# Optimization experiments

Hardware: AMD Instinct MI355X
Metric: run time of the kernel (lower is better)

The kernel has to match this reference:

```python
import jax, jax.numpy as jnp
import numpy as np

H = 4  # num_heads

def _ln(x, g, b):
    m = x.mean(-1, keepdims=True)
    v = ((x - m) ** 2).mean(-1, keepdims=True)
    return (x - m) * jax.lax.rsqrt(v + 1e-5) * g + b

def _mlp(x, w1, b1, w2, b2):
    return jax.nn.relu(x @ w1 + b1) @ w2 + b2

def _lin_att(q, k, v):
    # q,k,v: [BB, L, H, hd] ; linear (kernelized) attention, no softmax
    L = q.shape[1]
    qn = q / jnp.maximum(jnp.linalg.norm(q, axis=-1, keepdims=True), 1e-12)
    kn = k / jnp.maximum(jnp.linalg.norm(k, axis=-1, keepdims=True), 1e-12)
    kvs = jnp.einsum('blhm,blhd->bhmd', kn, v)
    num = jnp.einsum('bnhm,bhmd->bnhd', qn, kvs) + L * v
    den = jnp.einsum('bnhm,bhm->bnh', qn, kn.sum(axis=1))[..., None] + L
    return num / den

def _fast_attn(x4, w_qkv, w_op, b_op):
    # x4: [B,T,N,D]; spatial attention over N, temporal attention over T, concat, project
    B, T, N, D = x4.shape
    hd = D // H
    q, k, v = jnp.split(x4 @ w_qkv, 3, axis=-1)
    sh = lambda t: t.reshape(B * T, N, H, hd)
    out_s = _lin_att(sh(q), sh(k), sh(v)).reshape(B, T, N, D)
    th = lambda t: jnp.swapaxes(t, 1, 2).reshape(B * N, T, H, hd)
    out_t = jnp.swapaxes(_lin_att(th(q), th(k), th(v)).reshape(B, N, T, D), 1, 2)
    return jnp.concatenate([out_s, out_t], axis=-1) @ w_op + b_op

def _forward(x, W_in, b_in, adp, W_tp, b_tp, qkv_w, op_w, op_b, pw_w, pw_b,
             fc_w1, fc_b1, fc_w2, fc_b2, ln1_g, ln1_b, ln2_g, ln2_b,
             ep_w, ep_b, enc_w1, enc_b1, enc_w2, enc_b2, out_w, out_b):
    Nn, T, _ = x.shape
    xt = jnp.swapaxes(x, 0, 1)[None]                 # [1,T,N,in]
    h = xt @ W_in + b_in                             # input_proj -> [1,T,N,24]
    h = jnp.concatenate([h, adp[None]], axis=-1)     # + adaptive emb -> [1,T,N,104]
    h = h @ W_tp + b_tp                              # temporal_proj: 1x1 conv == pointwise linear
    graph = jnp.einsum('tnd,tmd->tnm', adp, adp)     # [T,N,N]
    graph = jax.nn.softmax(jax.nn.relu(graph), axis=-1)  # AvgPool(1,1) is identity
    # GraphPropagate (order=2, eval/no-dropout): [h, graph @ h]
    z1 = jnp.einsum('tni,btid->btnd', graph, h)
    att0 = _fast_attn(h, qkv_w[0], op_w[0], op_b[0])
    att1 = _fast_attn(z1, qkv_w[1], op_w[1], op_b[1])
    # scale = [1, 0.01]; note torch's in-place aliasing makes ln1 input = 2*x_glo
    g = h + att0 * (h @ pw_w[0] + pw_b[0]) + 0.01 * att1 * (att0 @ pw_w[1] + pw_b[1])
    h1 = _ln(2.0 * g, ln1_g, ln1_b)
    h2 = _ln(h1 + _mlp(h1, fc_w1, fc_b1, fc_w2, fc_b2), ln2_g, ln2_b)
    y = jnp.swapaxes(h2, 1, 2).reshape(1, Nn, T * h2.shape[-1]) @ ep_w + ep_b  # encoder_proj
    for i in range(enc_w1.shape[0]):                 # 3 residual MLP blocks
        y = y + _mlp(y, enc_w1[i], enc_b1[i], enc_w2[i], enc_b2[i])
    out = y @ out_w + out_b                          # [1,N,365]
    return out.reshape(Nn, T, 1)

def setup_inputs() -> dict:
    key = jax.random.key(0)
    ks = jax.random.split(key, 24)
    f = lambda i, shape, s=0.05: jax.random.normal(ks[i], shape, dtype=jnp.float32) * s
    D, T, N, IN = 104, 365, 400, 3
    return {
        'x': jax.random.normal(ks[0], (N, T, IN), dtype=jnp.float32),
        'W_in': f(1, (IN, 24)), 'b_in': f(2, (24,)),
        'adp': f(3, (T, N, 80)),
        'W_tp': f(4, (D, D)), 'b_tp': f(5, (D,)),
        'qkv_w': f(6, (2, D, 3 * D)),
        'op_w': f(7, (2, 2 * D, D)), 'op_b': f(8, (2, D)),
        'pw_w': f(9, (2, D, D)), 'pw_b': f(10, (2, D)),
        'fc_w1': f(11, (D, 2 * D)), 'fc_b1': f(12, (2 * D,)),
        'fc_w2': f(13, (2 * D, D)), 'fc_b2': f(14, (D,)),
        'ln1_g': jnp.ones((D,), jnp.float32), 'ln1_b': jnp.zeros((D,), jnp.float32),
        'ln2_g': jnp.ones((D,), jnp.float32), 'ln2_b': jnp.zeros((D,), jnp.float32),
        'ep_w': f(15, (T * D, D), 0.01), 'ep_b': f(16, (D,)),
        'enc_w1': f(17, (3, D, 2 * D)), 'enc_b1': f(18, (3, 2 * D)),
        'enc_w2': f(19, (3, 2 * D, D)), 'enc_b2': f(20, (3, D)),
        'out_w': f(21, (D, T)), 'out_b': f(22, (T,)),
    }

def reference(x, W_in, b_in, adp, W_tp, b_tp, qkv_w, op_w, op_b, pw_w, pw_b,
              fc_w1, fc_b1, fc_w2, fc_b2, ln1_g, ln1_b, ln2_g, ln2_b,
              ep_w, ep_b, enc_w1, enc_b1, enc_w2, enc_b2, out_w, out_b):
    return _forward(x, W_in, b_in, adp, W_tp, b_tp, qkv_w, op_w, op_b, pw_w, pw_b,
                    fc_w1, fc_b1, fc_w2, fc_b2, ln1_g, ln1_b, ln2_g, ln2_b,
                    ep_w, ep_b, enc_w1, enc_b1, enc_w2, enc_b2, out_w, out_b)
```

## Files before the change

### kernel.cpp

```cpp
#include <hip/hip_runtime.h>
#include <hip/hip_bf16.h>
#include <cstddef>

#define TT   365
#define NN   400
#define TN   (TT*NN)
#define HD   26
#define NH   4

#define CEILDIV(a,b) (((a)+(b)-1)/(b))

typedef __hip_bfloat16 bf16;
typedef short short8v __attribute__((ext_vector_type(8)));
typedef float float4v __attribute__((ext_vector_type(4)));
typedef float float16v __attribute__((ext_vector_type(16)));
__device__ __forceinline__ float b2f(bf16 v){ return __bfloat162float(v); }
__device__ __forceinline__ bf16  f2b(float v){ return __float2bfloat16(v); }

static constexpr size_t NB0 = (size_t)TN*104;
static constexpr size_t NB1 = (size_t)TN*104;
static constexpr size_t NB2 = (size_t)TN*312;
static constexpr size_t NB3 = (size_t)TN*104;
static constexpr size_t NBF = NB0+NB1+NB2+NB3;
static constexpr size_t NTILE   = (size_t)108*32;
// ... 190 lines not shown
    int m0 = blockIdx.x * 64;
    int tid = threadIdx.x;
    int lane = tid & 63, w = tid >> 6, n16 = lane & 15, quad = lane >> 4;
    uint4 z4 = {0u,0u,0u,0u};

    for (int idx = tid; idx < 64*16; idx += 256) {
        int r = idx >> 4, q = idx & 15;
        int m = m0 + r;
        uint4 v0 = z4, v1 = z4;
        if (m < TN && q < 13) {
            v0 = *(const uint4*)(h    + (size_t)m*104 + q*8);
            v1 = *(const uint4*)(att0 + (size_t)m*104 + q*8);
        }
        *(uint4*)(&A0s[r*STR + q*8]) = v0;
        *(uint4*)(&A1s[r*STR + q*8]) = v1;
    }
    for (int idx = tid; idx < 112*16; idx += 256) {
        int c = idx >> 4, q = idx & 15;
        uint4 v = z4;
        if (c < 104) v = *(const uint4*)(w0t + (size_t)c*128 + q*8);
        *(uint4*)(&Ws[c*STR + q*8]) = v;
    }
    for (int i = tid; i < 416; i += 256)
        prm[i] = (i < 208) ? pwb[i] : (i < 312 ? gamma[i-208] : beta[i-312]);
    __syncthreads();

    short8v a0f[4], a1f[4];
    #pragma unroll
    for (int s = 0; s < 4; ++s) {
        a0f[s] = *(const short8v*)(&A0s[(16*w + n16)*STR + s*32 + quad*8]);
        a1f[s] = *(const short8v*)(&A1s[(16*w + n16)*STR + s*32 + quad*8]);
    }
    float4v acc0[7], acc1[7];
    #pragma unroll
    for (int ct = 0; ct < 7; ++ct) { float4v z = {0.f,0.f,0.f,0.f}; acc0[ct] = z; acc1[ct] = z; }
    #pragma unroll
    for (int ct = 0; ct < 7; ++ct)
        #pragma unroll
        for (int s = 0; s < 4; ++s) {
            short8v bfr = *(const short8v*)(&Ws[(ct*16 + n16)*STR + s*32 + quad*8]);
            acc0[ct] = __builtin_amdgcn_mfma_f32_16x16x32_bf16(a0f[s], bfr, acc0[ct], 0, 0, 0);
        }
    __syncthreads();
    for (int idx = tid; idx < 112*16; idx += 256) {
        int c = idx >> 4, q = idx & 15;
        uint4 v = z4;
        if (c < 104) v = *(const uint4*)(w1t + (size_t)c*128 + q*8);
        *(uint4*)(&Ws[c*STR + q*8]) = v;
    }
    __syncthreads();
    #pragma unroll
    for (int ct = 0; ct < 7; ++ct)
        #pragma unroll
        for (int s = 0; s < 4; ++s) {
            short8v bfr = *(const short8v*)(&Ws[(ct*16 + n16)*STR + s*32 + quad*8]);
            acc1[ct] = __builtin_amdgcn_mfma_f32_16x16x32_bf16(a1f[s], bfr, acc1[ct], 0, 0, 0);
        }

    float sum[4] = {0.f,0.f,0.f,0.f};
    #pragma unroll
    for (int ct = 0; ct < 7; ++ct) {
        int c = ct*16 + n16;
        bool colok = c < 104;
        float b0 = colok ? prm[c] : 0.f;
        float b1 = colok ? prm[104 + c] : 0.f;
        #pragma unroll
        for (int reg = 0; reg < 4; ++reg) {
            int r = 16*w + quad*4 + reg;
            int m = m0 + r;
            float xv = 0.f;
            if (colok && m < TN) {
                float p0 = acc0[ct][reg] + b0;
                float p1 = acc1[ct][reg] + b1;
                float hv = b2f(A0s[r*STR + c]);
                float a0 = b2f(A1s[r*STR + c]);
                float a1 = b2f(att1[(size_t)m*104 + c]);
                xv = 2.f*(hv + a0*p0 + 0.01f*a1*p1);
            }
            acc0[ct][reg] = xv;
            sum[reg] += xv;
        }
    }
    #pragma unroll
    for (int reg = 0; reg < 4; ++reg) {
        float v = sum[reg];
        v += __shfl_xor(v,1,64); v += __shfl_xor(v,2,64);
        v += __shfl_xor(v,4,64); v += __shfl_xor(v,8,64);
        sum[reg] = v * (1.f/104.f);
    }
    float var[4] = {0.f,0.f,0.f,0.f};
    #pragma unroll
    for (int ct = 0; ct < 7; ++ct) {
        bool colok = (ct*16 + n16) < 104;
        #pragma unroll
        for (int reg = 0; reg < 4; ++reg) {
            if (colok) {
                float d = acc0[ct][reg] - sum[reg];
                acc0[ct][reg] = d;
                var[reg] += d*d;
            }
        }
    }
    #pragma unroll
    for (int reg = 0; reg < 4; ++reg) {
        float v = var[reg];
        v += __shfl_xor(v,1,64); v += __shfl_xor(v,2,64);
        v += __shfl_xor(v,4,64); v += __shfl_xor(v,8,64);
        var[reg] = rsqrtf(v * (1.f/104.f) + 1e-5f);
    }
    #pragma unroll
    for (int ct = 0; ct < 7; ++ct) {
        int c = ct*16 + n16;
        if (c < 104) {
            float g = prm[208 + c], be = prm[312 + c];
            #pragma unroll
            for (int reg = 0; reg < 4; ++reg) {
                int m = m0 + 16*w + quad*4 + reg;
                if (m < TN)
                    h[(size_t)m*104 + c] = f2b(acc0[ct][reg]*var[reg]*g + be);
            }
        }
    }
}

__global__ void __launch_bounds__(256) fc2_ln2(
    const bf16* __restrict__ hidden, const bf16* __restrict__ w2t, const float* __restrict__ b2,
    const bf16* __restrict__ h1, const float* __restrict__ gamma, const float* __restrict__ beta,
    bf16* __restrict__ h2)
{
    constexpr int STRA = 232;
    constexpr int STRW = 136;
    __shared__ bf16 As[64*STRA];
    __shared__ bf16 Ws[112*STRW];
    __shared__ float prm[312];
    int m0 = blockIdx.x * 64;
    int tid = threadIdx.x;
    int lane = tid & 63, w = tid >> 6, n16 = lane & 15, quad = lane >> 4;
    uint4 z4 = {0u,0u,0u,0u};

    for (int idx = tid; idx < 64*28; idx += 256) {
        int r = idx / 28, q = idx - r*28;
        int m = m0 + r;
        uint4 v = z4;
        if (m < TN && q < 26) v = *(const uint4*)(hidden + (size_t)m*208 + q*8);
        *(uint4*)(&As[r*STRA + q*8]) = v;
    }
    for (int idx = tid; idx < 112*16; idx += 256) {
        int c = idx >> 4, q = idx & 15;
        uint4 v = z4;
        if (c < 104) v = *(const uint4*)(w2t + (size_t)c*224 + q*8);
        *(uint4*)(&Ws[c*STRW + q*8]) = v;
    }
    for (int i = tid; i < 312; i += 256)
        prm[i] = (i < 104) ? b2[i] : (i < 208 ? gamma[i-104] : beta[i-208]);
    __syncthreads();

    short8v af[7];
    #pragma unroll
    for (int s = 0; s < 7; ++s)
        af[s] = *(const short8v*)(&As[(16*w + n16)*STRA + s*32 + quad*8]);
    float4v acc[7];
    #pragma unroll
    for (int ct = 0; ct < 7; ++ct) { float4v z = {0.f,0.f,0.f,0.f}; acc[ct] = z; }
    #pragma unroll
    for (int ct = 0; ct < 7; ++ct)
        #pragma unroll
        for (int s = 0; s < 4; ++s) {
            short8v bfr = *(const short8v*)(&Ws[(ct*16 + n16)*STRW + s*32 + quad*8]);
            acc[ct] = __builtin_amdgcn_mfma_f32_16x16x32_bf16(af[s], bfr, acc[ct], 0, 0, 0);
        }
    __syncthreads();
    for (int idx = tid; idx < 112*16; idx += 256) {
        int c = idx >> 4, q = idx & 15;
        uint4 v = z4;
        if (c < 104 && q < 12) v = *(const uint4*)(w2t + (size_t)c*224 + 128 + q*8);
        *(uint4*)(&Ws[c*STRW + q*8]) = v;
    }
    __syncthreads();
    #pragma unroll
    for (int ct = 0; ct < 7; ++ct)
        #pragma unroll
        for (int s = 4; s < 7; ++s) {
            short8v bfr = *(const short8v*)(&Ws[(ct*16 + n16)*STRW + (s-4)*32 + quad*8]);
            acc[ct] = __builtin_amdgcn_mfma_f32_16x16x32_bf16(af[s], bfr, acc[ct], 0, 0, 0);
        }

    float sum[4] = {0.f,0.f,0.f,0.f};
    #pragma unroll
    for (int ct = 0; ct < 7; ++ct) {
        int c = ct*16 + n16;
        bool colok = c < 104;
        float bb = colok ? prm[c] : 0.f;
        #pragma unroll
        for (int reg = 0; reg < 4; ++reg) {
            int m = m0 + 16*w + quad*4 + reg;
            float xv = 0.f;
            if (colok && m < TN)
                xv = b2f(h1[(size_t)m*104 + c]) + acc[ct][reg] + bb;
            acc[ct][reg] = xv;
            sum[reg] += xv;
        }
    }
    #pragma unroll
    for (int reg = 0; reg < 4; ++reg) {
        float v = sum[reg];
        v += __shfl_xor(v,1,64); v += __shfl_xor(v,2,64);
        v += __shfl_xor(v,4,64); v += __shfl_xor(v,8,64);
        sum[reg] = v * (1.f/104.f);
    }
    float var[4] = {0.f,0.f,0.f,0.f};
    #pragma unroll
    for (int ct = 0; ct < 7; ++ct) {
        bool colok = (ct*16 + n16) < 104;
        #pragma unroll
        for (int reg = 0; reg < 4; ++reg) {
            if (colok) {
                float d = acc[ct][reg] - sum[reg];
                acc[ct][reg] = d;
                var[reg] += d*d;
            }
        }
    }
    #pragma unroll
    for (int reg = 0; reg < 4; ++reg) {
        float v = var[reg];
        v += __shfl_xor(v,1,64); v += __shfl_xor(v,2,64);
        v += __shfl_xor(v,4,64); v += __shfl_xor(v,8,64);
        var[reg] = rsqrtf(v * (1.f/104.f) + 1e-5f);
    }
    #pragma unroll
    for (int ct = 0; ct < 7; ++ct) {
        int c = ct*16 + n16;
        if (c < 104) {
            float g = prm[104 + c], be = prm[208 + c];
            #pragma unroll
            for (int reg = 0; reg < 4; ++reg) {
                int m = m0 + 16*w + quad*4 + reg;
                if (m < TN)
                    h2[(size_t)m*104 + c] = f2b(acc[ct][reg]*var[reg]*g + be);
            }
        }
    }
}

__global__ void __launch_bounds__(256) ep_mf(
    const bf16* __restrict__ h2, const bf16* __restrict__ wt, float* __restrict__ y)
{
    constexpr int STR = 136;
    __shared__ bf16 As[64*STR];
    __shared__ bf16 Ws[64*STR];
    int m0 = blockIdx.x * 64;
    int c0 = blockIdx.y * 64;
    int t0 = blockIdx.z * 8;
    int t1 = min(TT, t0 + 8);
    int tid = threadIdx.x;
    int lane = tid & 63, w = tid >> 6, n16 = lane & 15, quad = lane >> 4;
    uint4 z4 = {0u,0u,0u,0u};

    float4v acc[4];
    #pragma unroll
    for (int ct = 0; ct < 4; ++ct) { float4v z = {0.f,0.f,0.f,0.f}; acc[ct] = z; }

    for (int t = t0; t < t1; ++t) {
        for (int idx = tid; idx < 64*16; idx += 256) {
            int r = idx >> 4, q = idx & 15;
            int m = m0 + r;
            uint4 va = z4;
            if (m < NN && q < 13) va = *(const uint4*)(h2 + ((size_t)t*NN + m)*104 + q*8);
            *(uint4*)(&As[r*STR + q*8]) = va;
            int c = c0 + r;
            uint4 vw = z4;
            if (c < 104 && q < 13) vw = *(const uint4*)(wt + (size_t)c*37960 + t*104 + q*8);
            *(uint4*)(&Ws[r*STR + q*8]) = vw;
        }
        __syncthreads();
        short8v af[4];
        #pragma unroll
        for (int s = 0; s < 4; ++s)
            af[s] = *(const short8v*)(&As[(16*w + n16)*STR + s*32 + quad*8]);
        #pragma unroll
        for (int ct = 0; ct < 4; ++ct) {
            #pragma unroll
            for (int s = 0; s < 4; ++s) {
                short8v bfr = *(const short8v*)(&Ws[(ct*16 + n16)*STR + s*32 + quad*8]);
                acc[ct] = __builtin_amdgcn_mfma_f32_16x16x32_bf16(af[s], bfr, acc[ct], 0, 0, 0);
            }
        }
        __syncthreads();
    }
    #pragma unroll
    for (int ct = 0; ct < 4; ++ct) {
        int c = c0 + ct*16 + n16;
        if (c < 104) {
            #pragma unroll
            for (int reg = 0; reg < 4; ++reg) {
                int m = m0 + 16*w + quad*4 + reg;
                if (m < NN) atomicAdd(&y[(size_t)m*104 + c], acc[ct][reg]);
            }
        }
    }
}

static constexpr int Z1_TQ = CEILDIV(TT, 8);
static constexpr int Z1_BLOCKS = 8 * Z1_TQ * 7;
__global__ void __launch_bounds__(256, 3) z1_mf(
    const bf16* __restrict__ adp_bf, const bf16* __restrict__ hT, bf16* __restrict__ z1)
{
    constexpr int SA  = 104;
    constexpr int SPH = 72;
    constexpr int SPP = 72;
    __shared__ bf16 Bt[64*SA];
    __shared__ bf16 Hs[128*SPH];
    __shared__ bf16 P [64*SPP];
    __shared__ float rsb[2][64];
    bf16* As = Hs;

    int bid = blockIdx.x;
    int xcd = bid & 7;
    int j = bid >> 3;
    int tq = j / 7, rblk = j - tq*7;
    int t = tq*8 + xcd;
    if (t >= TT) return;
    int r0 = rblk*64;

    int tid = threadIdx.x;
    int lane = tid & 63, w = tid >> 6;
    int n32 = lane & 31, koct = lane >> 5;
    int qi = w >> 1, ci = w & 1;

    {
        const uint4* src = (const uint4*)(adp_bf + ((size_t)t*NN + r0)*96);
        for (int idx = tid; idx < 768; idx += 256) {
            int r = idx / 12, q = idx - r*12;
            *(uint4*)(&As[r*SA + q*8]) = src[idx];
        }
    }
    __syncthreads();
    short8v af2[6];
    #pragma unroll
    for (int s = 0; s < 6; ++s)
        af2[s] = *(const short8v*)(&As[(qi*32 + n32)*SA + s*16 + koct*8]);
    __syncthreads();
    {
        uint4 z4v = {0u,0u,0u,0u};
        for (int idx = tid; idx < 216; idx += 256) {
            int r = 104 + idx/9, q = idx - (idx/9)*9;
            *(uint4*)(&Hs[r*SPH + q*8]) = z4v;
        }
    }

    float16v onum0, onum1;
    #pragma unroll
    for (int i = 0; i < 16; ++i) { onum0[i] = 0.f; onum1[i] = 0.f; }
    float rs2[16];
    #pragma unroll
    for (int i = 0; i < 16; ++i) rs2[i] = 0.f;

    uint4 preB[3], preH[4];
    {
        const uint4* srcB = (const uint4*)(adp_bf + (size_t)t*NN*96);
        #pragma unroll
        for (int j2 = 0; j2 < 3; ++j2) preB[j2] = srcB[tid + j2*256];
        const bf16* hb = hT + (size_t)t*104*448;
        #pragma unroll
        for (int j2 = 0; j2 < 4; ++j2) {
            int idx = tid + j2*256;
            uint4 v = {0u,0u,0u,0u};
            if (idx < 832) {
                int d = idx >> 3, q = idx & 7;
                v = *(const uint4*)(hb + (size_t)d*448 + q*8);
            }
            preH[j2] = v;
        }
    }

    for (int c0 = 0; c0 < NN; c0 += 64) {
        #pragma unroll
        for (int j2 = 0; j2 < 3; ++j2) {
            int idx = tid + j2*256;
            int r = idx / 12, q = idx - r*12;
            *(uint4*)(&Bt[r*SA + q*8]) = preB[j2];
        }
        #pragma unroll
        for (int j2 = 0; j2 < 4; ++j2) {
            int idx = tid + j2*256;
            if (idx < 832) {
                int d = idx >> 3, q = idx & 7;
                *(uint4*)(&Hs[d*SPH + q*8]) = preH[j2];
            }
        }
        __syncthreads();
        int cn = c0 + 64;
        if (cn < NN) {
            const uint4* srcB = (const uint4*)(adp_bf + ((size_t)t*NN + cn)*96);
            #pragma unroll
            for (int j2 = 0; j2 < 3; ++j2) preB[j2] = srcB[tid + j2*256];
            const bf16* hb = hT + (size_t)t*104*448 + cn;
            #pragma unroll
            for (int j2 = 0; j2 < 4; ++j2) {
                int idx = tid + j2*256;
                if (idx < 832) {
                    int d = idx >> 3, q = idx & 7;
                    preH[j2] = *(const uint4*)(hb + (size_t)d*448 + q*8);
                }
            }
        }
        float16v sc;
        #pragma unroll
        for (int i = 0; i < 16; ++i) sc[i] = 0.f;
        #pragma unroll
        for (int s = 0; s < 6; ++s) {
            short8v bfr = *(const short8v*)(&Bt[(ci*32 + n32)*SA + s*16 + koct*8]);
            sc = __builtin_amdgcn_mfma_f32_32x32x16_bf16(af2[s], bfr, sc, 0, 0, 0);
        }
        bool colok = (c0 + ci*32 + n32) < NN;
        #pragma unroll
        for (int reg = 0; reg < 16; ++reg) {
            int crow = (reg & 3) + 8*(reg >> 2) + 4*koct;
            float e = colok ? __expf(fmaxf(sc[reg], 0.f)) : 0.f;
            rs2[reg] += e;
            P[(qi*32 + crow)*SPP + ci*32 + n32] = f2b(e);
        }
        __syncthreads();
        short8v pA[4];
        #pragma unroll
        for (int s = 0; s < 4; ++s)
            pA[s] = *(const short8v*)(&P[(qi*32 + n32)*SPP + s*16 + koct*8]);
        int dt0 = (w & 1), dt1 = dt0 + 2;
        #pragma unroll
        for (int s = 0; s < 4; ++s) {
            short8v hb0 = *(const short8v*)(&Hs[(dt0*32 + n32)*SPH + s*16 + koct*8]);
            onum0 = __builtin_amdgcn_mfma_f32_32x32x16_bf16(pA[s], hb0, onum0, 0, 0, 0);
        }
        #pragma unroll
        for (int s = 0; s < 4; ++s) {
            short8v hb1 = *(const short8v*)(&Hs[(dt1*32 + n32)*SPH + s*16 + koct*8]);
            onum1 = __builtin_amdgcn_mfma_f32_32x32x16_bf16(pA[s], hb1, onum1, 0, 0, 0);
        }
        __syncthreads();
    }

    #pragma unroll
    for (int reg = 0; reg < 16; ++reg) {
        float v = rs2[reg];
        v += __shfl_xor(v, 1, 64);
        v += __shfl_xor(v, 2, 64);
        v += __shfl_xor(v, 4, 64);
        v += __shfl_xor(v, 8, 64);
        v += __shfl_xor(v, 16, 64);
        if (n32 == 0) {
            int crow = (reg & 3) + 8*(reg >> 2) + 4*koct;
            rsb[ci][qi*32 + crow] = v;
        }
    }
    __syncthreads();

    int dt0 = (w & 1), dt1 = dt0 + 2;
    #pragma unroll
    for (int reg = 0; reg < 16; ++reg) {
        int crow = (reg & 3) + 8*(reg >> 2) + 4*koct;
        int qrow = qi*32 + crow;
        int gq = r0 + qrow;
        if (gq < NN) {
            float inv = 1.f / (rsb[0][qrow] + rsb[1][qrow]);
            int d0 = dt0*32 + n32;
            z1[((size_t)t*NN + gq)*104 + d0] = f2b(onum0[reg] * inv);
            int d1 = dt1*32 + n32;
            if (d1 < 104)
                z1[((size_t)t*NN + gq)*104 + d1] = f2b(onum1[reg] * inv);
        }
    }
}

__global__ void __launch_bounds__(256) kvs_mf(
    const bf16* __restrict__ qkv, bf16* __restrict__ kvsb_s, bf16* __restrict__ kvsb_t)
{
    constexpr int CK = 32;
    constexpr int TS = 40;
    __shared__ bf16 raw[CK][216];
    __shared__ bf16 kTn[4][32][TS];
    __shared__ bf16 vT [4][32][TS];
    __shared__ float invs[CK][4];

    int bb = blockIdx.x;
    bf16* out; int L; long long strideL, base;
    if (bb < TT) { out = kvsb_s + (size_t)bb*NTILE; L = NN; base = (long long)bb*NN*312 + 104; strideL = 312; }
    else { int n = bb - TT; out = kvsb_t + (size_t)n*NTILE; L = TT; base = (long long)n*312 + 104; strideL = (long long)NN*312; }

    int tid = threadIdx.x;
    int lane = tid & 63, w = tid >> 6;
    int n32 = lane & 31, koct = lane >> 5;
    uint4 z4 = {0u,0u,0u,0u};

    float16v acc;
    #pragma unroll
    for (int i = 0; i < 16; ++i) acc[i] = 0.f;

    uint4 pre[4];
    #pragma unroll
    for (int j = 0; j < 4; ++j) {
        int idx = tid + j*256;
        uint4 v = z4;
        if (idx < CK*26) {
            int r = idx / 26, q = idx - r*26;
            if (r < L) v = *(const uint4*)(qkv + base + (long long)r*strideL + q*8);
        }
        pre[j] = v;
    }

    for (int l0 = 0; l0 < L; l0 += CK) {
        int lw = min(CK, L - l0);
        __syncthreads();
        #pragma unroll
        for (int j = 0; j < 4; ++j) {
            int idx = tid + j*256;
            if (idx < CK*26) {
                int r = idx / 26, q = idx - r*26;
                *(uint4*)(&raw[r][q*8]) = pre[j];
            }
        }
        __syncthreads();
        {
            int ln0 = l0 + CK;
            #pragma unroll
            for (int j = 0; j < 4; ++j) {
                int idx = tid + j*256;
                uint4 v = z4;
                if (idx < CK*26 && ln0 < L) {
                    int r = idx / 26, q = idx - r*26;
                    if (r < L - ln0) v = *(const uint4*)(qkv + base + (long long)(ln0 + r)*strideL + q*8);
                }
                pre[j] = v;
            }
        }
        if (tid < CK*4) {
            int l = tid >> 2, h = tid & 3;
            float ss = 0.f;
            #pragma unroll
            for (int m = 0; m < HD; ++m) { float v = b2f(raw[l][h*HD + m]); ss += v*v; }
            invs[l][h] = (l < lw) ? 1.f/fmaxf(sqrtf(ss), 1e-12f) : 0.f;
        }
        __syncthreads();
        for (int idx = tid; idx < 4*CK*HD; idx += 256) {
            int h = idx / (CK*HD); int rem = idx - h*CK*HD;
            int l = rem / HD; int m = rem - l*HD;
            float iv = invs[l][h];
            kTn[h][m][l] = f2b(b2f(raw[l][h*HD + m]) * iv);
            vT[h][m][l]  = raw[l][104 + h*HD + m];
        }
        if (tid < 4*CK) {
            int h = tid >> 5, l = tid & 31;
            vT[h][26][l] = f2b((l < lw) ? 1.f : 0.f);
        }
        __syncthreads();
        #pragma unroll
        for (int s = 0; s < 2; ++s) {
            short8v a = *(const short8v*)(&kTn[w][n32][s*16 + koct*8]);
            short8v b = *(const short8v*)(&vT [w][n32][s*16 + koct*8]);
            acc = __builtin_amdgcn_mfma_f32_32x32x16_bf16(a, b, acc, 0, 0, 0);
        }
    }

    int lo = w*HD;
    #pragma unroll
    for (int reg = 0; reg < 16; ++reg) {
        int m = (reg & 3) + 8*(reg >> 2) + 4*koct;
        if (m < HD) {
            if (n32 < HD)       out[(size_t)(lo + n32)*32 + m] = f2b(acc[reg]);
            else if (n32 == HD) out[(size_t)(104 + w)*32 + m] = f2b(acc[reg]);
        }
    }
}

__global__ void __launch_bounds__(256) attn_mm(
    bf16* __restrict__ qkv, const bf16* __restrict__ kvsb,
    int M, long long bStride, long long rowStride, float Lf, int outOff)
{
    constexpr int STR = 136;
    __shared__ bf16 As[64*STR];
    __shared__ bf16 Ws[112*STR];
    __shared__ float nsqL[64*4];
    __shared__ float denL[64*4];
    int mt = blockIdx.x, bb = blockIdx.y;
    int tid = threadIdx.x;
    int lane = tid & 63, w = tid >> 6, n16 = lane & 15, quad = lane >> 4;
    bf16* base = qkv + (size_t)bb * bStride;
    int r0 = mt*64;
    uint4 z4 = {0u,0u,0u,0u};

    for (int idx = tid; idx < 64*16; idx += 256) {
        int r = idx >> 4, q = idx & 15;
        int m = r0 + r;
        uint4 v = z4;
        if (m < M && q < 13) v = *(const uint4*)(base + (size_t)m*rowStride + q*8);
        *(uint4*)(&As[r*STR + q*8]) = v;
    }
    for (int idx = tid; idx < 112*16; idx += 256) {
        int c = idx >> 4, q = idx & 15;
        *(uint4*)(&Ws[c*STR + q*8]) = z4;
    }
    __syncthreads();
    {
        const bf16* kb = kvsb + (size_t)bb * NTILE;
        for (int idx = tid; idx < 108*13; idx += 256) {
            int c = idx / 13, qu = idx - c*13;
            int lo = (c < 104) ? (c/26)*26 : (c-104)*26;
            *(uint*)(&Ws[c*STR + lo + qu*2]) = *(const uint*)(kb + (size_t)c*32 + qu*2);
        }
    }
    __syncthreads();

    short8v af[4];
    #pragma unroll
    for (int s = 0; s < 4; ++s)
        af[s] = *(const short8v*)(&As[(16*w + n16)*STR + s*32 + quad*8]);
    float4v acc[7];
    #pragma unroll
    for (int ct = 0; ct < 7; ++ct) { float4v z = {0.f,0.f,0.f,0.f}; acc[ct] = z; }
    #pragma unroll
    for (int ct = 0; ct < 7; ++ct) {
        #pragma unroll
        for (int s = 0; s < 4; ++s) {
            short8v bfr = *(const short8v*)(&Ws[(ct*16 + n16)*STR + s*32 + quad*8]);
            acc[ct] = __builtin_amdgcn_mfma_f32_16x16x32_bf16(af[s], bfr, acc[ct], 0, 0, 0);
        }
    }
    {
        int row = tid >> 2, hh = tid & 3;
        const bf16* qr = &As[row*STR + hh*26];
        float ss = 0.f;
        #pragma unroll
        for (int m = 0; m < HD; ++m) { float v = b2f(qr[m]); ss += v*v; }
        nsqL[row*4 + hh] = ss;
    }
    if (n16 >= 8 && n16 < 12) {
        #pragma unroll
        for (int reg = 0; reg < 4; ++reg)
            denL[(16*w + quad*4 + reg)*4 + (n16 - 8)] = acc[6][reg];
    }
    __syncthreads();
    #pragma unroll
    for (int ct = 0; ct < 7; ++ct) {
        int c = ct*16 + n16;
        if (c < 104) {
            int hh = c / 26;
            #pragma unroll
            for (int reg = 0; reg < 4; ++reg) {
                int lr = 16*w + quad*4 + reg;
                int m = r0 + lr;
                if (m < M) {
                    float iq = 1.f / fmaxf(sqrtf(nsqL[lr*4 + hh]), 1e-12f);
                    float den = iq * denL[lr*4 + hh] + Lf;
                    bf16* rp = base + (size_t)m*rowStride;
                    float num = iq * acc[ct][reg] + Lf * b2f(rp[208 + c]);
                    rp[outOff + c] = f2b(num / den);
                }
            }
        }
    }
}

__global__ void __launch_bounds__(256) y_init_kernel(float* __restrict__ y, const float* __restrict__ ep_b) {
    int i = blockIdx.x*256 + threadIdx.x;
    if (i < NN*104) y[i] = ep_b[i % 104];
}

__global__ void __launch_bounds__(256) enc_kernel(
    float* __restrict__ y, const float* __restrict__ w1, const float* __restrict__ b1,
    const float* __restrict__ w2, const float* __restrict__ b2)
{
    int n = blockIdx.x;
    int tid = threadIdx.x;
    __shared__ float yr[104], hid[208];
    if (tid < 104) yr[tid] = y[(size_t)n*104 + tid];
    __syncthreads();
    if (tid < 208) {
        float s = b1[tid];
        for (int k = 0; k < 104; ++k) s += yr[k] * w1[(size_t)k*208 + tid];
        hid[tid] = fmaxf(s, 0.f);
    }
    __syncthreads();
    if (tid < 104) {
        float s = b2[tid];
        for (int k = 0; k < 208; ++k) s += hid[k] * w2[(size_t)k*104 + tid];
        y[(size_t)n*104 + tid] = yr[tid] + s;
    }
}

__global__ void __launch_bounds__(256) out_kernel(
    const float* __restrict__ y, const float* __restrict__ out_w,
    const float* __restrict__ out_b, float* __restrict__ out)
{
    int n = blockIdx.x;
    int tid = threadIdx.x;
    __shared__ float yr[104];
    if (tid < 104) yr[tid] = y[(size_t)n*104 + tid];
    __syncthreads();
    for (int t = tid; t < TT; t += 256) {
        float s = out_b[t];
        for (int d = 0; d < 104; ++d) s += yr[d] * out_w[(size_t)d*TT + t];
        out[(size_t)n*TT + t] = s;
    }
}

extern "C" void kernel_launch(void* const* d_in, const int* in_sizes, int n_in,
                              void* d_out, int out_size, void* d_ws, size_t ws_size,
                              hipStream_t stream) {
    if (ws_size < WS_NEEDED) return;

    const float* x      = (const float*)d_in[0];
    const float* W_in   = (const float*)d_in[1];
    const float* b_in   = (const float*)d_in[2];
    const float* adp    = (const float*)d_in[3];
    const float* W_tp   = (const float*)d_in[4];
    const float* b_tp   = (const float*)d_in[5];
    const float* qkv_w  = (const float*)d_in[6];
    const float* op_w   = (const float*)d_in[7];
    const float* op_b   = (const float*)d_in[8];
    const float* pw_w   = (const float*)d_in[9];
    const float* pw_b   = (const float*)d_in[10];
    const float* fc_w1  = (const float*)d_in[11];
    const float* fc_b1  = (const float*)d_in[12];
    const float* fc_w2  = (const float*)d_in[13];
    const float* fc_b2  = (const float*)d_in[14];
    const float* ln1_g  = (const float*)d_in[15];
    const float* ln1_b  = (const float*)d_in[16];
    const float* ln2_g  = (const float*)d_in[17];
    const float* ln2_b  = (const float*)d_in[18];
    const float* ep_w   = (const float*)d_in[19];
    const float* ep_b   = (const float*)d_in[20];
    const float* enc_w1 = (const float*)d_in[21];
    const float* enc_b1 = (const float*)d_in[22];
    const float* enc_w2 = (const float*)d_in[23];
    const float* enc_b2 = (const float*)d_in[24];
    const float* out_w  = (const float*)d_in[25];
    const float* out_b  = (const float*)d_in[26];

    bf16* B0 = (bf16*)d_ws;
    bf16* B1 = B0 + NB0;
    bf16* B2 = B1 + NB1;
    bf16* B3 = B2 + NB2;
    bf16* kvsb_s = B3 + NB3;
    bf16* kvsb_t = kvsb_s + NKVSB_S;
    float* ybuf  = (float*)(kvsb_t + NKVSB_T);
    bf16* wtp   = (bf16*)(ybuf + NY);
    bf16* wqkv0 = wtp + NW_TP;
    bf16* wqkv1 = wqkv0 + NW_QKV;
    bf16* wop0  = wqkv1 + NW_QKV;
    bf16* wop1  = wop0 + NW_OP;
    bf16* wpw0  = wop1 + NW_OP;
    bf16* wpw1  = wpw0 + NW_PW;
    bf16* wfc1  = wpw1 + NW_PW;
    bf16* wfc2  = wfc1 + NW_FC1;
    bf16* wept  = wfc2 + NW_FC2;
    bf16* adp_bf = B2;
    bf16* hTbuf  = B2 + NADP;

    prep_w<<<CEILDIV(104*128,256), 256, 0, stream>>>(W_tp, wtp, 104, 104, 128);
    prep_w<<<CEILDIV(312*128,256), 256, 0, stream>>>(qkv_w, wqkv0, 104, 312, 128);
    prep_w<<<CEILDIV(312*128,256), 256, 0, stream>>>(qkv_w + 104*312, wqkv1, 104, 312, 128);
    prep_w<<<CEILDIV(104*224,256), 256, 0, stream>>>(op_w, wop0, 208, 104, 224);
    prep_w<<<CEILDIV(104*224,256), 256, 0, stream>>>(op_w + 208*104, wop1, 208, 104, 224);
    prep_w<<<CEILDIV(104*128,256), 256, 0, stream>>>(pw_w, wpw0, 104, 104, 128);
    prep_w<<<CEILDIV(104*128,256), 256, 0, stream>>>(pw_w + 104*104, wpw1, 104, 104, 128);
    prep_w<<<CEILDIV(208*128,256), 256, 0, stream>>>(fc_w1, wfc1, 104, 208, 128);
    prep_w<<<CEILDIV(104*224,256), 256, 0, stream>>>(fc_w2, wfc2, 208, 104, 224);
    prep_wT<<<CEILDIV(37960,64), 256, 0, stream>>>(ep_w, wept);

    const int GX = CEILDIV(TN, 64);

    hcat_kernel<<<TN, 128, 0, stream>>>(x, W_in, b_in, adp, B2);
    gemm_mf<128><<<GX*2, 256, 0, stream>>>(B2, 104, 104, wtp, b_tp, B0, TN, 104, 0);
    prep_adp<<<CEILDIV((int)NADP,256), 256, 0, stream>>>(adp, adp_bf);
    ht_kernel<<<dim3(7, TT), 256, 0, stream>>>(B0, hTbuf);
    z1_mf<<<Z1_BLOCKS, 256, 0, stream>>>(adp_bf, hTbuf, B1);
    gemm_mf<128><<<GX*5, 256, 0, stream>>>(B0, 104, 104, wqkv0, nullptr, B2, TN, 312, 0);
    kvs_mf<<<TT+NN, 256, 0, stream>>>(B2, kvsb_s, kvsb_t);
    attn_mm<<<dim3(6, NN), 256, 0, stream>>>(B2, kvsb_t, TT, 312, (long long)NN*312, (float)TT, 104);
    attn_mm<<<dim3(7, TT), 256, 0, stream>>>(B2, kvsb_s, NN, (long long)NN*312, 312, (float)NN, 0);
    gemm_mf<224><<<GX*2, 256, 0, stream>>>(B2, 312, 208, wop0, op_b, B3, TN, 104, 0);
    gemm_mf<128><<<GX*5, 256, 0, stream>>>(B1, 104, 104, wqkv1, nullptr, B2, TN, 312, 0);
    kvs_mf<<<TT+NN, 256, 0, stream>>>(B2, kvsb_s, kvsb_t);
    attn_mm<<<dim3(6, NN), 256, 0, stream>>>(B2, kvsb_t, TT, 312, (long long)NN*312, (float)TT, 104);
    attn_mm<<<dim3(7, TT), 256, 0, stream>>>(B2, kvsb_s, NN, (long long)NN*312, 312, (float)NN, 0);
    gemm_mf<224><<<GX*2, 256, 0, stream>>>(B2, 312, 208, wop1, op_b + 104, B1, TN, 104, 0);
    gate_ln1<<<GX, 256, 0, stream>>>(B0, B3, B1, wpw0, wpw1, pw_b, ln1_g, ln1_b);
    gemm_mf<128><<<GX*4, 256, 0, stream>>>(B0, 104, 104, wfc1, fc_b1, B2, TN, 208, 1);
    fc2_ln2<<<GX, 256, 0, stream>>>(B2, wfc2, fc_b2, B0, ln2_g, ln2_b, B3);
    y_init_kernel<<<CEILDIV(NN*104,256), 256, 0, stream>>>(ybuf, ep_b);
    ep_mf<<<dim3(CEILDIV(NN,64), 2, CEILDIV(TT,8)), 256, 0, stream>>>(B3, wept, ybuf);
    for (int i = 0; i < 3; ++i)
        enc_kernel<<<NN, 256, 0, stream>>>(ybuf, enc_w1 + (size_t)i*104*208, enc_b1 + (size_t)i*208,
                                           enc_w2 + (size_t)i*208*104, enc_b2 + (size_t)i*104);
    out_kernel<<<NN, 256, 0, stream>>>(ybuf, out_w, out_b, (float*)d_out);
}
```

Baseline: 1.320 ms.

## Split z1 graph-propagate kernel over feature halves and keep P in registers

The z1 kernel now splits the 104-wide output feature dimension into two halves across separate blocks, doubling the grid and raising the occupancy hint to 4. The score MFMA is transposed so the exp'd probabilities can be packed to bf16 and rearranged with permlane32 swaps directly into A-operand registers. This removes the P round-trip through LDS and one barrier per tile. Waves now split the key dimension and reduce partial outputs through shared memory at the end. The cost is recomputing the QK^T scores and exponentials twice (once per half).

```diff
diff --git a/kernel.cpp b/kernel.cpp
--- a/kernel.cpp
+++ b/kernel.cpp
@@ -516,22 +516,23 @@
 }
 
 static constexpr int Z1_TQ = CEILDIV(TT, 8);
-static constexpr int Z1_BLOCKS = 8 * Z1_TQ * 7;
-__global__ void __launch_bounds__(256, 3) z1_mf(
+static constexpr int Z1_BLOCKS = 8 * Z1_TQ * 7 * 2;
+__global__ void __launch_bounds__(256, 4) z1_mf(
     const bf16* __restrict__ adp_bf, const bf16* __restrict__ hT, bf16* __restrict__ z1)
 {
-    constexpr int SA  = 104;
-    constexpr int SPH = 72;
-    constexpr int SPP = 72;
-    __shared__ bf16 Bt[64*SA];
-    __shared__ bf16 Hs[128*SPH];
-    __shared__ bf16 P [64*SPP];
-    __shared__ float rsb[2][64];
-    bf16* As = Hs;
+    constexpr int SA = 104;
+    constexpr int SH = 72;
+    __shared__ __align__(16) bf16 lds[64*SA*2 + 64*SH];
+    __shared__ float rsbp[128];
+    bf16* Asq = lds;
+    bf16* Bt  = lds + 64*SA;
+    bf16* Hs  = lds + 128*SA;
+    float* xbuf = (float*)lds;
 
     int bid = blockIdx.x;
     int xcd = bid & 7;
     int j = bid >> 3;
+    int dh = j & 1; j >>= 1;
     int tq = j / 7, rblk = j - tq*7;
     int t = tq*8 + xcd;
     if (t >= TT) return;
@@ -546,44 +547,29 @@
         const uint4* src = (const uint4*)(adp_bf + ((size_t)t*NN + r0)*96);
         for (int idx = tid; idx < 768; idx += 256) {
             int r = idx / 12, q = idx - r*12;
-            *(uint4*)(&As[r*SA + q*8]) = src[idx];
-        }
-    }
-    __syncthreads();
-    short8v af2[6];
-    #pragma unroll
-    for (int s = 0; s < 6; ++s)
-        af2[s] = *(const short8v*)(&As[(qi*32 + n32)*SA + s*16 + koct*8]);
-    __syncthreads();
-    {
-        uint4 z4v = {0u,0u,0u,0u};
-        for (int idx = tid; idx < 216; idx += 256) {
-            int r = 104 + idx/9, q = idx - (idx/9)*9;
-            *(uint4*)(&Hs[r*SPH + q*8]) = z4v;
-        }
-    }
-
-    float16v onum0, onum1;
-    #pragma unroll
-    for (int i = 0; i < 16; ++i) { onum0[i] = 0.f; onum1[i] = 0.f; }
-    float rs2[16];
-    #pragma unroll
-    for (int i = 0; i < 16; ++i) rs2[i] = 0.f;
-
-    uint4 preB[3], preH[4];
+            *(uint4*)(&Asq[r*SA + q*8]) = src[idx];
+        }
+    }
+
+    float16v on0, on1;
+    #pragma unroll
+    for (int i = 0; i < 16; ++i) { on0[i] = 0.f; on1[i] = 0.f; }
+    float rs = 0.f;
+
+    const bf16* hbase = hT + (size_t)t*104*448 + (size_t)(dh*64)*448;
+    const int hrows = (dh == 0) ? 64 : 40;
+
+    uint4 preB[3], preH[2];
     {
         const uint4* srcB = (const uint4*)(adp_bf + (size_t)t*NN*96);
         #pragma unroll
         for (int j2 = 0; j2 < 3; ++j2) preB[j2] = srcB[tid + j2*256];
-        const bf16* hb = hT + (size_t)t*104*448;
-        #pragma unroll
-        for (int j2 = 0; j2 < 4; ++j2) {
+        #pragma unroll
+        for (int j2 = 0; j2 < 2; ++j2) {
             int idx = tid + j2*256;
+            int r = idx >> 3, c8 = idx & 7;
             uint4 v = {0u,0u,0u,0u};
-            if (idx < 832) {
-                int d = idx >> 3, q = idx & 7;
-                v = *(const uint4*)(hb + (size_t)d*448 + q*8);
-            }
+            if (r < hrows) v = *(const uint4*)(hbase + (size_t)r*448 + c8*8);
             preH[j2] = v;
         }
     }
@@ -596,12 +582,10 @@
             *(uint4*)(&Bt[r*SA + q*8]) = preB[j2];
         }
         #pragma unroll
-        for (int j2 = 0; j2 < 4; ++j2) {
+        for (int j2 = 0; j2 < 2; ++j2) {
             int idx = tid + j2*256;
-            if (idx < 832) {
-                int d = idx >> 3, q = idx & 7;
-                *(uint4*)(&Hs[d*SPH + q*8]) = preH[j2];
-            }
+            int r = idx >> 3, c8 = idx & 7;
+            *(uint4*)(&Hs[r*SH + c8*8]) = preH[j2];
         }
         __syncthreads();
         int cn = c0 + 64;
@@ -609,14 +593,13 @@
             const uint4* srcB = (const uint4*)(adp_bf + ((size_t)t*NN + cn)*96);
             #pragma unroll
             for (int j2 = 0; j2 < 3; ++j2) preB[j2] = srcB[tid + j2*256];
-            const bf16* hb = hT + (size_t)t*104*448 + cn;
             #pragma unroll
-            for (int j2 = 0; j2 < 4; ++j2) {
+            for (int j2 = 0; j2 < 2; ++j2) {
                 int idx = tid + j2*256;
-                if (idx < 832) {
-                    int d = idx >> 3, q = idx & 7;
-                    preH[j2] = *(const uint4*)(hb + (size_t)d*448 + q*8);
-                }
+                int r = idx >> 3, c8 = idx & 7;
+                uint4 v = {0u,0u,0u,0u};
+                if (r < hrows) v = *(const uint4*)(hbase + (size_t)r*448 + cn + c8*8);
+                preH[j2] = v;
             }
         }
         float16v sc;
@@ -624,64 +607,66 @@
         for (int i = 0; i < 16; ++i) sc[i] = 0.f;
         #pragma unroll
         for (int s = 0; s < 6; ++s) {
-            short8v bfr = *(const short8v*)(&Bt[(ci*32 + n32)*SA + s*16 + koct*8]);
-            sc = __builtin_amdgcn_mfma_f32_32x32x16_bf16(af2[s], bfr, sc, 0, 0, 0);
-        }
-        bool colok = (c0 + ci*32 + n32) < NN;
+            short8v afc = *(const short8v*)(&Bt [(ci*32 + n32)*SA + s*16 + koct*8]);
+            short8v bq  = *(const short8v*)(&Asq[(qi*32 + n32)*SA + s*16 + koct*8]);
+            sc = __builtin_amdgcn_mfma_f32_32x32x16_bf16(afc, bq, sc, 0, 0, 0);
+        }
+        uint r8[8];
+        #pragma unroll
+        for (int i = 0; i < 8; ++i) {
+            int crow0 = (2*i & 3) + 8*(2*i >> 2) + 4*koct;
+            int cg = c0 + ci*32 + crow0;
+            float e0 = (cg     < NN) ? __expf(fmaxf(sc[2*i],   0.f)) : 0.f;
+            float e1 = (cg + 1 < NN) ? __expf(fmaxf(sc[2*i+1], 0.f)) : 0.f;
+            rs += e0 + e1;
+            asm("v_cvt_pk_bf16_f32 %0, %1, %2" : "=v"(r8[i]) : "v"(e0), "v"(e1));
+        }
+        asm volatile("v_permlane32_swap_b32 %0, %1" : "+v"(r8[2]), "+v"(r8[0]));
+        asm volatile("v_permlane32_swap_b32 %0, %1" : "+v"(r8[3]), "+v"(r8[1]));
+        asm volatile("v_permlane32_swap_b32 %0, %1" : "+v"(r8[6]), "+v"(r8[4]));
+        asm volatile("v_permlane32_swap_b32 %0, %1" : "+v"(r8[7]), "+v"(r8[5]));
+        union { uint4 u; short8v s; } cv0, cv1;
+        cv0.u.x = r8[0]; cv0.u.y = r8[1]; cv0.u.z = r8[2]; cv0.u.w = r8[3];
+        cv1.u.x = r8[4]; cv1.u.y = r8[5]; cv1.u.z = r8[6]; cv1.u.w = r8[7];
+        #pragma unroll
+        for (int s = 0; s < 2; ++s) {
+            short8v pa = (s == 0) ? cv0.s : cv1.s;
+            short8v h0 = *(const short8v*)(&Hs[(0*32 + n32)*SH + ci*32 + s*16 + koct*8]);
+            on0 = __builtin_amdgcn_mfma_f32_32x32x16_bf16(pa, h0, on0, 0, 0, 0);
+            short8v h1 = *(const short8v*)(&Hs[(1*32 + n32)*SH + ci*32 + s*16 + koct*8]);
+            on1 = __builtin_amdgcn_mfma_f32_32x32x16_bf16(pa, h1, on1, 0, 0, 0);
+        }
+        __syncthreads();
+    }
+
+    float rsl = rs + __shfl_xor(rs, 32, 64);
+    if (koct == 0) rsbp[ci*64 + qi*32 + n32] = rsl;
+    if (ci == 1) {
         #pragma unroll
         for (int reg = 0; reg < 16; ++reg) {
             int crow = (reg & 3) + 8*(reg >> 2) + 4*koct;
-            float e = colok ? __expf(fmaxf(sc[reg], 0.f)) : 0.f;
-            rs2[reg] += e;
-            P[(qi*32 + crow)*SPP + ci*32 + n32] = f2b(e);
-        }
-        __syncthreads();
-        short8v pA[4];
-        #pragma unroll
-        for (int s = 0; s < 4; ++s)
-            pA[s] = *(const short8v*)(&P[(qi*32 + n32)*SPP + s*16 + koct*8]);
-        int dt0 = (w & 1), dt1 = dt0 + 2;
-        #pragma unroll
-        for (int s = 0; s < 4; ++s) {
-            short8v hb0 = *(const short8v*)(&Hs[(dt0*32 + n32)*SPH + s*16 + koct*8]);
-            onum0 = __builtin_amdgcn_mfma_f32_32x32x16_bf16(pA[s], hb0, onum0, 0, 0, 0);
-        }
-        #pragma unroll
-        for (int s = 0; s < 4; ++s) {
-            short8v hb1 = *(const short8v*)(&Hs[(dt1*32 + n32)*SPH + s*16 + koct*8]);
-            onum1 = __builtin_amdgcn_mfma_f32_32x32x16_bf16(pA[s], hb1, onum1, 0, 0, 0);
-        }
-        __syncthreads();
-    }
-
-    #pragma unroll
-    for (int reg = 0; reg < 16; ++reg) {
-        float v = rs2[reg];
-        v += __shfl_xor(v, 1, 64);
-        v += __shfl_xor(v, 2, 64);
-        v += __shfl_xor(v, 4, 64);
-        v += __shfl_xor(v, 8, 64);
-        v += __shfl_xor(v, 16, 64);
-        if (n32 == 0) {
+            xbuf[qi*2048 +        crow*32 + n32] = on0[reg];
+            xbuf[qi*2048 + 1024 + crow*32 + n32] = on1[reg];
+        }
+    }
+    __syncthreads();
+    if (ci == 0) {
+        float rtot = rsbp[qi*32 + n32] + rsbp[64 + qi*32 + n32];
+        float inv = 1.f / rtot;
+        #pragma unroll
+        for (int reg = 0; reg < 16; ++reg) {
             int crow = (reg & 3) + 8*(reg >> 2) + 4*koct;
-            rsb[ci][qi*32 + crow] = v;
-        }
-    }
-    __syncthreads();
-
-    int dt0 = (w & 1), dt1 = dt0 + 2;
-    #pragma unroll
-    for (int reg = 0; reg < 16; ++reg) {
-        int crow = (reg & 3) + 8*(reg >> 2) + 4*koct;
-        int qrow = qi*32 + crow;
-        int gq = r0 + qrow;
-        if (gq < NN) {
-            float inv = 1.f / (rsb[0][qrow] + rsb[1][qrow]);
-            int d0 = dt0*32 + n32;
-            z1[((size_t)t*NN + gq)*104 + d0] = f2b(onum0[reg] * inv);
-            int d1 = dt1*32 + n32;
-            if (d1 < 104)
-                z1[((size_t)t*NN + gq)*104 + d1] = f2b(onum1[reg] * inv);
+            int gq = r0 + qi*32 + crow;
+            if (gq < NN) {
+                float v0 = (on0[reg] + xbuf[qi*2048 + crow*32 + n32]) * inv;
+                int d0 = dh*64 + n32;
+                z1[((size_t)t*NN + gq)*104 + d0] = f2b(v0);
+                int d1 = dh*64 + 32 + n32;
+                if (d1 < 104) {
+                    float v1 = (on1[reg] + xbuf[qi*2048 + 1024 + crow*32 + n32]) * inv;
+                    z1[((size_t)t*NN + gq)*104 + d1] = f2b(v1);
+                }
+            }
         }
     }
 }
```

Result: slower. 1.384 ms (+4.8%).

## Process two query slabs per z1 block to share adjacency and H tiles

Applied to the files above, without the earlier changes.

The graph-propagation kernel z1_mf now runs 512 threads per block covering two 64-row query slabs. Both slabs share each streamed key-side adjacency tile (Bt) and H tile, so global loads and LDS staging of those tiles are halved per output row. Query-side A fragments now sit in LDS and are re-read every iteration instead of staying in registers. The grid changes from 7 row blocks to 4 row pairs per timestep, so the last pair includes one slab that lies entirely past NN; its work is wasted and its A load reads past the row range.

```diff
diff --git a/kernel.cpp b/kernel.cpp
--- a/kernel.cpp
+++ b/kernel.cpp
@@ -516,116 +516,100 @@
 }
 
 static constexpr int Z1_TQ = CEILDIV(TT, 8);
-static constexpr int Z1_BLOCKS = 8 * Z1_TQ * 7;
-__global__ void __launch_bounds__(256, 3) z1_mf(
+static constexpr int Z1_BLOCKS = 8 * Z1_TQ * 4;
+__global__ void __launch_bounds__(512, 4) z1_mf(
     const bf16* __restrict__ adp_bf, const bf16* __restrict__ hT, bf16* __restrict__ z1)
 {
     constexpr int SA  = 104;
-    constexpr int SPH = 72;
+    constexpr int SH  = 72;
     constexpr int SPP = 72;
+    __shared__ bf16 Asq[2][64*SA];
     __shared__ bf16 Bt[64*SA];
-    __shared__ bf16 Hs[128*SPH];
-    __shared__ bf16 P [64*SPP];
-    __shared__ float rsb[2][64];
-    bf16* As = Hs;
+    __shared__ bf16 Hs[128*SH];
+    __shared__ bf16 P[2][64*SPP];
+    __shared__ float rsb[2][2][64];
 
     int bid = blockIdx.x;
     int xcd = bid & 7;
     int j = bid >> 3;
-    int tq = j / 7, rblk = j - tq*7;
+    int tq = j >> 2, pair = j & 3;
     int t = tq*8 + xcd;
     if (t >= TT) return;
-    int r0 = rblk*64;
 
     int tid = threadIdx.x;
     int lane = tid & 63, w = tid >> 6;
+    int slab = w >> 2, wsl = w & 3;
+    int qi = wsl >> 1, ci = wsl & 1;
     int n32 = lane & 31, koct = lane >> 5;
-    int qi = w >> 1, ci = w & 1;
+    int r0 = (pair*2 + slab)*64;
 
     {
-        const uint4* src = (const uint4*)(adp_bf + ((size_t)t*NN + r0)*96);
-        for (int idx = tid; idx < 768; idx += 256) {
-            int r = idx / 12, q = idx - r*12;
-            *(uint4*)(&As[r*SA + q*8]) = src[idx];
-        }
-    }
-    __syncthreads();
-    short8v af2[6];
-    #pragma unroll
-    for (int s = 0; s < 6; ++s)
-        af2[s] = *(const short8v*)(&As[(qi*32 + n32)*SA + s*16 + koct*8]);
-    __syncthreads();
+        const uint4* src = (const uint4*)(adp_bf + ((size_t)t*NN + pair*128)*96);
+        #pragma unroll
+        for (int i = 0; i < 3; ++i) {
+            int idx = tid + i*512;
+            int s2 = idx / 768, rem = idx - s2*768;
+            int r = rem / 12, q = rem - r*12;
+            *(uint4*)(&Asq[s2][r*SA + q*8]) = src[idx];
+        }
+    }
     {
         uint4 z4v = {0u,0u,0u,0u};
-        for (int idx = tid; idx < 216; idx += 256) {
-            int r = 104 + idx/9, q = idx - (idx/9)*9;
-            *(uint4*)(&Hs[r*SPH + q*8]) = z4v;
-        }
-    }
-
-    float16v onum0, onum1;
-    #pragma unroll
-    for (int i = 0; i < 16; ++i) { onum0[i] = 0.f; onum1[i] = 0.f; }
+        for (int idx = tid; idx < 216; idx += 512) {
+            int rr = idx / 9;
+            int r = 104 + rr, q = idx - rr*9;
+            *(uint4*)(&Hs[r*SH + q*8]) = z4v;
+        }
+    }
+
+    float16v on0, on1;
+    #pragma unroll
+    for (int i = 0; i < 16; ++i) { on0[i] = 0.f; on1[i] = 0.f; }
     float rs2[16];
     #pragma unroll
     for (int i = 0; i < 16; ++i) rs2[i] = 0.f;
 
-    uint4 preB[3], preH[4];
+    const bf16* hbase = hT + (size_t)t*104*448;
+
+    uint4 preB0, preB1, preH0, preH1;
     {
         const uint4* srcB = (const uint4*)(adp_bf + (size_t)t*NN*96);
-        #pragma unroll
-        for (int j2 = 0; j2 < 3; ++j2) preB[j2] = srcB[tid + j2*256];
-        const bf16* hb = hT + (size_t)t*104*448;
-        #pragma unroll
-        for (int j2 = 0; j2 < 4; ++j2) {
-            int idx = tid + j2*256;
-            uint4 v = {0u,0u,0u,0u};
-            if (idx < 832) {
-                int d = idx >> 3, q = idx & 7;
-                v = *(const uint4*)(hb + (size_t)d*448 + q*8);
-            }
-            preH[j2] = v;
-        }
+        preB0 = srcB[tid];
+        if (tid < 256) preB1 = srcB[tid + 512];
+        { int r = tid >> 3, q = tid & 7;
+          preH0 = *(const uint4*)(hbase + (size_t)r*448 + q*8); }
+        if (tid < 320) { int idx = tid + 512; int r = idx >> 3, q = idx & 7;
+          preH1 = *(const uint4*)(hbase + (size_t)r*448 + q*8); }
     }
 
     for (int c0 = 0; c0 < NN; c0 += 64) {
-        #pragma unroll
-        for (int j2 = 0; j2 < 3; ++j2) {
-            int idx = tid + j2*256;
-            int r = idx / 12, q = idx - r*12;
-            *(uint4*)(&Bt[r*SA + q*8]) = preB[j2];
-        }
-        #pragma unroll
-        for (int j2 = 0; j2 < 4; ++j2) {
-            int idx = tid + j2*256;
-            if (idx < 832) {
-                int d = idx >> 3, q = idx & 7;
-                *(uint4*)(&Hs[d*SPH + q*8]) = preH[j2];
-            }
-        }
+        { int r = tid / 12, q = tid - (tid/12)*12;
+          *(uint4*)(&Bt[r*SA + q*8]) = preB0; }
+        if (tid < 256) { int idx = tid + 512; int r = idx / 12, q = idx - r*12;
+          *(uint4*)(&Bt[r*SA + q*8]) = preB1; }
+        { int r = tid >> 3, q = tid & 7;
+          *(uint4*)(&Hs[r*SH + q*8]) = preH0; }
+        if (tid < 320) { int idx = tid + 512; int r = idx >> 3, q = idx & 7;
+          *(uint4*)(&Hs[r*SH + q*8]) = preH1; }
         __syncthreads();
         int cn = c0 + 64;
         if (cn < NN) {
             const uint4* srcB = (const uint4*)(adp_bf + ((size_t)t*NN + cn)*96);
-            #pragma unroll
-            for (int j2 = 0; j2 < 3; ++j2) preB[j2] = srcB[tid + j2*256];
-            const bf16* hb = hT + (size_t)t*104*448 + cn;
-            #pragma unroll
-            for (int j2 = 0; j2 < 4; ++j2) {
-                int idx = tid + j2*256;
-                if (idx < 832) {
-                    int d = idx >> 3, q = idx & 7;
-                    preH[j2] = *(const uint4*)(hb + (size_t)d*448 + q*8);
-                }
-            }
+            preB0 = srcB[tid];
+            if (tid < 256) preB1 = srcB[tid + 512];
+            { int r = tid >> 3, q = tid & 7;
+              preH0 = *(const uint4*)(hbase + (size_t)r*448 + cn + q*8); }
+            if (tid < 320) { int idx = tid + 512; int r = idx >> 3, q = idx & 7;
+              preH1 = *(const uint4*)(hbase + (size_t)r*448 + cn + q*8); }
         }
         float16v sc;
         #pragma unroll
         for (int i = 0; i < 16; ++i) sc[i] = 0.f;
         #pragma unroll
         for (int s = 0; s < 6; ++s) {
+            short8v afq = *(const short8v*)(&Asq[slab][(qi*32 + n32)*SA + s*16 + koct*8]);
             short8v bfr = *(const short8v*)(&Bt[(ci*32 + n32)*SA + s*16 + koct*8]);
-            sc = __builtin_amdgcn_mfma_f32_32x32x16_bf16(af2[s], bfr, sc, 0, 0, 0);
+            sc = __builtin_amdgcn_mfma_f32_32x32x16_bf16(afq, bfr, sc, 0, 0, 0);
         }
         bool colok = (c0 + ci*32 + n32) < NN;
         #pragma unroll
@@ -633,23 +617,22 @@
             int crow = (reg & 3) + 8*(reg >> 2) + 4*koct;
             float e = colok ? __expf(fmaxf(sc[reg], 0.f)) : 0.f;
             rs2[reg] += e;
-            P[(qi*32 + crow)*SPP + ci*32 + n32] = f2b(e);
+            P[slab][(qi*32 + crow)*SPP + ci*32 + n32] = f2b(e);
         }
         __syncthreads();
         short8v pA[4];
         #pragma unroll
         for (int s = 0; s < 4; ++s)
-            pA[s] = *(const short8v*)(&P[(qi*32 + n32)*SPP + s*16 + koct*8]);
-        int dt0 = (w & 1), dt1 = dt0 + 2;
+            pA[s] = *(const short8v*)(&P[slab][(qi*32 + n32)*SPP + s*16 + koct*8]);
         #pragma unroll
         for (int s = 0; s < 4; ++s) {
-            short8v hb0 = *(const short8v*)(&Hs[(dt0*32 + n32)*SPH + s*16 + koct*8]);
-            onum0 = __builtin_amdgcn_mfma_f32_32x32x16_bf16(pA[s], hb0, onum0, 0, 0, 0);
+            short8v hb0 = *(const short8v*)(&Hs[(ci*32 + n32)*SH + s*16 + koct*8]);
+            on0 = __builtin_amdgcn_mfma_f32_32x32x16_bf16(pA[s], hb0, on0, 0, 0, 0);
         }
         #pragma unroll
         for (int s = 0; s < 4; ++s) {
-            short8v hb1 = *(const short8v*)(&Hs[(dt1*32 + n32)*SPH + s*16 + koct*8]);
-            onum1 = __builtin_amdgcn_mfma_f32_32x32x16_bf16(pA[s], hb1, onum1, 0, 0, 0);
+            short8v hb1 = *(const short8v*)(&Hs[((ci+2)*32 + n32)*SH + s*16 + koct*8]);
+            on1 = __builtin_amdgcn_mfma_f32_32x32x16_bf16(pA[s], hb1, on1, 0, 0, 0);
         }
         __syncthreads();
     }
@@ -664,24 +647,23 @@
         v += __shfl_xor(v, 16, 64);
         if (n32 == 0) {
             int crow = (reg & 3) + 8*(reg >> 2) + 4*koct;
-            rsb[ci][qi*32 + crow] = v;
-        }
-    }
-    __syncthreads();
-
-    int dt0 = (w & 1), dt1 = dt0 + 2;
+            rsb[slab][ci][qi*32 + crow] = v;
+        }
+    }
+    __syncthreads();
+
     #pragma unroll
     for (int reg = 0; reg < 16; ++reg) {
         int crow = (reg & 3) + 8*(reg >> 2) + 4*koct;
         int qrow = qi*32 + crow;
         int gq = r0 + qrow;
         if (gq < NN) {
-            float inv = 1.f / (rsb[0][qrow] + rsb[1][qrow]);
-            int d0 = dt0*32 + n32;
-            z1[((size_t)t*NN + gq)*104 + d0] = f2b(onum0[reg] * inv);
-            int d1 = dt1*32 + n32;
+            float inv = 1.f / (rsb[slab][0][qrow] + rsb[slab][1][qrow]);
+            int d0 = ci*32 + n32;
+            z1[((size_t)t*NN + gq)*104 + d0] = f2b(on0[reg] * inv);
+            int d1 = (ci + 2)*32 + n32;
             if (d1 < 104)
-                z1[((size_t)t*NN + gq)*104 + d1] = f2b(onum1[reg] * inv);
+                z1[((size_t)t*NN + gq)*104 + d1] = f2b(on1[reg] * inv);
         }
     }
 }
@@ -987,7 +969,7 @@
     gemm_mf<128><<<GX*2, 256, 0, stream>>>(B2, 104, 104, wtp, b_tp, B0, TN, 104, 0);
     prep_adp<<<CEILDIV((int)NADP,256), 256, 0, stream>>>(adp, adp_bf);
     ht_kernel<<<dim3(7, TT), 256, 0, stream>>>(B0, hTbuf);
-    z1_mf<<<Z1_BLOCKS, 256, 0, stream>>>(adp_bf, hTbuf, B1);
+    z1_mf<<<Z1_BLOCKS, 512, 0, stream>>>(adp_bf, hTbuf, B1);
     gemm_mf<128><<<GX*5, 256, 0, stream>>>(B0, 104, 104, wqkv0, nullptr, B2, TN, 312, 0);
     kvs_mf<<<TT+NN, 256, 0, stream>>>(B2, kvsb_s, kvsb_t);
     attn_mm<<<dim3(6, NN), 256, 0, stream>>>(B2, kvsb_t, TT, 312, (long long)NN*312, (float)TT, 104);
```

Result: no change. 1.303 ms (-1.3%).
